# Performance work log

Hardware: AMD Instinct MI355X
Metric: run time of the kernel (lower is better)

Reference implementation:

```python
import jax, jax.numpy as jnp
import numpy as np

B, K, U = 4096, 512, 3
P, LIFT, HID, NSUB = 5, 32, 128, 10
RATE_LO, RATE_HI = 0.01, 3.0
BASAL_LO, BASAL_HI = 0.0, 0.3


def _xavier(key, shape):
    fan_in, fan_out = shape[1], shape[0]
    lim = np.sqrt(6.0 / (fan_in + fan_out))
    return jax.random.uniform(key, shape, jnp.float32, -lim, lim)


def setup_inputs() -> dict:
    key = jax.random.key(0)
    ks = jax.random.split(key, 10)
    return {
        "y0": jax.random.uniform(ks[0], (B, P), jnp.float32),
        "u_seq": jax.random.uniform(ks[1], (B, K, U), jnp.float32),
        "dt_seq": jax.random.uniform(ks[2], (B, K), jnp.float32),
        # lift: Linear(in_u+P -> LIFT)
        "Wl": _xavier(ks[3], (LIFT, U + P)),
        "bl": jnp.zeros((LIFT,), jnp.float32),
        # GRU (single layer): weight_ih (3H, LIFT), weight_hh (3H, H)
        "W_ih": _xavier(ks[4], (3 * HID, LIFT)),
        "b_ih": jnp.zeros((3 * HID,), jnp.float32),
        "W_hh": _xavier(ks[5], (3 * HID, HID)),
        "b_hh": jnp.zeros((3 * HID,), jnp.float32),
        # head: Linear(H -> 13)
        "Wh": _xavier(ks[6], (13, HID)),
        "bh": jnp.zeros((13,), jnp.float32),
        # bolus-to-state jump matrix (in_u, P)
        "u_to_y_jump": 0.1 * jax.random.uniform(ks[7], (U, P), jnp.float32),
    }


def _rhs(y, theta):
    # y: (B,5) [A,D,G,J,M]; theta: (B,13) [kf1..4, kr1..4, kj1..5]
    A, D, G, J, M = (y[:, i] for i in range(5))
    kf1, kf2, kf3, kf4, kr1, kr2, kr3, kr4, kj1, kj2, kj3, kj4, kj5 = (
        theta[:, i] for i in range(13))
    dA = -kf1 * A + kr1 * D + kj1
    dD = kf1 * A - kr1 * D - kf2 * D + kr2 * G + kj2
    dG = kf2 * D - kr2 * G - kf3 * G + kr3 * J + kj3
    dJ = kf3 * G - kr3 * J - kf4 * J + kr4 * M + kj4
    dM = kf4 * J - kr4 * M + kj5
    return jnp.stack([dA, dD, dG, dJ, dM], axis=-1)


def _rk4(y, h, theta):
    # h: (B,1) substep size
    k1 = _rhs(y, theta)
    k2 = _rhs(y + 0.5 * h * k1, theta)
    k3 = _rhs(y + 0.5 * h * k2, theta)
    k4 = _rhs(y + h * k3, theta)
    return jnp.maximum(y + h / 6.0 * (k1 + 2.0 * k2 + 2.0 * k3 + k4), 0.0)


def reference(y0, u_seq, dt_seq, Wl, bl, W_ih, b_ih, W_hh, b_hh, Wh, bh, u_to_y_jump):
    Bb = y0.shape[0]
    hid = W_hh.shape[1]

    def step(carry, inp):
        y_prev, hst = carry
        u_k, dt_k = inp  # (B,U), (B,)
        feat = jnp.concatenate([u_k, jax.lax.stop_gradient(y_prev)], axis=-1)
        x = jax.nn.silu(feat @ Wl.T + bl)
        # PyTorch GRUCell math
        gx = x @ W_ih.T + b_ih
        gh = hst @ W_hh.T + b_hh
        gxr, gxz, gxn = jnp.split(gx, 3, axis=-1)
        ghr, ghz, ghn = jnp.split(gh, 3, axis=-1)
        r = jax.nn.sigmoid(gxr + ghr)
        zg = jax.nn.sigmoid(gxz + ghz)
        n = jnp.tanh(gxn + r * ghn)
        h_new = (1.0 - zg) * n + zg * hst
        raw = h_new @ Wh.T + bh
        rates = RATE_LO + (RATE_HI - RATE_LO) * jax.nn.sigmoid(raw[:, 0:8])
        basal = BASAL_LO + (BASAL_HI - BASAL_LO) * jax.nn.sigmoid(raw[:, 8:13])
        theta = jnp.concatenate([rates, basal], axis=-1)
        y = y_prev + u_k @ u_to_y_jump
        hsub = (dt_k / float(NSUB))[:, None]
        for _ in range(NSUB):
            y = _rk4(y, hsub, theta)
        return (y, h_new), (y, theta)

    y_init = y0 + 0.01
    h0 = jnp.zeros((Bb, hid), dtype=y0.dtype)
    # scan over time: (K,B,...)
    _, (ys, thetas) = jax.lax.scan(
        step, (y_init, h0), (u_seq.transpose(1, 0, 2), dt_seq.T))
    y_out = ys.transpose(1, 0, 2)        # (B,K,P)
    theta_out = thetas.transpose(1, 0, 2)  # (B,K,13)
    return y_out, theta_out
```

## Files before the change

kernel.cpp:

```cpp
#include <hip/hip_runtime.h>
#include <cstdint>
#include <cstddef>


#define KTOT 512
#define BB   16

typedef _Float16 half8 __attribute__((ext_vector_type(8)));
typedef float    f32x4 __attribute__((ext_vector_type(4)));

struct __align__(16) Smem {
  _Float16 hf16[BB][136];
  _Float16 xls[BB][32];
  float yring[2][BB][16][5];
  float thring[2][BB][16][13];
  float brz[256];
  float bnx[128];
  float bnh[128];
  float bhv[16];
  float yst[BB][8];
  float ust[2][BB][4];
  float dtst[2][BB];
};

__device__ __forceinline__ float sigm(float x)     { return 1.f / (1.f + __expf(-x)); }
__device__ __forceinline__ float tanhfast(float x) { return 1.f - 2.f / (1.f + __expf(2.f * x)); }

template<int CTRL>
__device__ __forceinline__ float dppf(float x) {
  return __int_as_float(__builtin_amdgcn_mov_dpp(__float_as_int(x), CTRL, 0xf, 0xf, true));
}
#define QP_PLUS  0x39
#define QP_MINUS 0x93
#define QB0 0x00
#define QB1 0x55
#define QB2 0xAA
#define QB3 0xFF

#define MATMUL(Yr, Y4r, Xr, X4r, ALPHA) do {                                  \
  float xm_[5], xp_[5];                                                       \
  _Pragma("unroll")                                                           \
  for (int j_ = 0; j_ < 5; j_++) {                                            \
    xm_[j_] = dppf<QP_MINUS>(Xr[j_]);                                         \
    xp_[j_] = dppf<QP_PLUS >(Xr[j_]);                                         \
  }                                                                           \
  _Pragma("unroll")                                                           \
  for (int j_ = 0; j_ < 5; j_++) {                                            \
    const float ac_ = Zl*xm_[j_] + Zd*Xr[j_] + Zu*xp_[j_] + Zu4*X4r[j_];      \
    const float a4_ = Z43*Xr[j_] + Z44*X4r[j_];                               \
    Yr[j_]  = ((j_ == s_) ? 1.f : 0.f) + (ALPHA)*ac_;                         \
    Y4r[j_] = ((j_ == 4 ) ? 1.f : 0.f) + (ALPHA)*a4_;                         \
  } } while (0)

__global__ __launch_bounds__(512, 2) void rnn_scan_kernel(
    const float* __restrict__ y0,    const float* __restrict__ u_seq,
    const float* __restrict__ dt_sq, const float* __restrict__ Wl,
    const float* __restrict__ bl,    const float* __restrict__ W_ih,
    const float* __restrict__ b_ih,  const float* __restrict__ W_hh,
    const float* __restrict__ b_hh,  const float* __restrict__ Wh,
    const float* __restrict__ bh,    const float* __restrict__ jmp,
    float* __restrict__ y_out, float* __restrict__ th_out)
{
  __shared__ Smem sm;
  const int t   = threadIdx.x;
  const int w   = t >> 6;
  const int l   = t & 63;
  const int n16 = l & 15;
  const int q   = l >> 4;
  const int B0  = blockIdx.x * BB;

  if (t < 256) sm.brz[t] = b_ih[t] + b_hh[t];
  if (t < 128) { sm.bnx[t] = b_ih[256+t]; sm.bnh[t] = b_hh[256+t]; }
  if (t < 16)  sm.bhv[t] = (t < 13) ? bh[t] : 0.f;
  if (t >= 256 && t < 384) { const int b = (t-256) >> 3, i = (t-256) & 7;
    sm.yst[b][i] = (i < 5) ? (y0[(size_t)(B0+b)*5 + i] + 0.01f) : 0.f; }
  if (t >= 384 && t < 432) { const int idx = t-384, b = idx/3, c = idx - (idx/3)*3;
    sm.ust[0][b][c] = u_seq[((size_t)(B0+b)*KTOT + 0)*3 + c]; }
  if (t >= 432 && t < 448) sm.dtst[0][t-432] = dt_sq[(size_t)(B0+(t-432))*KTOT + 0];

  const int lb = t >> 5;
  const int lo = t & 31;
  float wlc[8];
  #pragma unroll
  for (int c = 0; c < 8; c++) wlc[c] = Wl[lo*8 + c];
  const float blv = bl[lo];

  half8 whf[4];
  #pragma unroll
  for (int ks = 0; ks < 4; ks++)
    #pragma unroll
    for (int i = 0; i < 8; i++) {
      const int kk = ks*32 + q*8 + i;
      whf[ks][i] = (n16 < 13) ? (_Float16)Wh[n16*128 + kk] : (_Float16)0.f;
    }

  const int jR = w*16 + n16;
  const int jZ = jR + 128, jN = jR + 256;
  half8 wihR, wihZ, wihN, whhR[4], whhZ[4], whhN[4];
  #pragma unroll
  for (int i = 0; i < 8; i++) {
    const int kk = q*8 + i;
    wihR[i] = (_Float16)W_ih[jR*32 + kk];
    wihZ[i] = (_Float16)W_ih[jZ*32 + kk];
    wihN[i] = (_Float16)W_ih[jN*32 + kk];
  }
  #pragma unroll
  for (int ks = 0; ks < 4; ks++)
    #pragma unroll
    for (int i = 0; i < 8; i++) {
      const int kk = ks*32 + q*8 + i;
      whhR[ks][i] = (_Float16)W_hh[jR*128 + kk];
      whhZ[ks][i] = (_Float16)W_hh[jZ*128 + kk];
      whhN[ks][i] = (_Float16)W_hh[jN*128 + kk];
    }

  float hreg[4] = {0.f, 0.f, 0.f, 0.f};
  const f32x4 zero4 = {0.f, 0.f, 0.f, 0.f};
  f32x4 accPreR = zero4, accPreZ = zero4, accPreN = zero4;

  const int s_ = l & 3, b4 = l >> 2;
  const float jr0 = jmp[0*5 + s_], jr1 = jmp[1*5 + s_], jr2 = jmp[2*5 + s_];
  const float j40 = (s_==3) ? jmp[4]  : 0.f;
  const float j41 = (s_==3) ? jmp[9]  : 0.f;
  const float j42 = (s_==3) ? jmp[14] : 0.f;

  const int upb = l/3, upc = l - (l/3)*3;

  __syncthreads();

  const float br  = sm.brz[jR];
  const float bz  = sm.brz[128 + jR];
  const float bx  = sm.bnx[jR];
  const float bn  = sm.bnh[jR];
  const float bb_ = sm.bhv[n16];

  #pragma unroll 1
  for (int k = 0; k < KTOT; k++) {
    const int buf  = k & 1;
    const int nbuf = (k + 1) & 1;
    const int kp   = (k + 1 < KTOT) ? (k + 1) : (KTOT - 1);

    {
      const f32x4 uu = *(const f32x4*)&sm.ust[buf][lb][0];
      const f32x4 ya = *(const f32x4*)&sm.yst[lb][0];
      const f32x4 yc = *(const f32x4*)&sm.yst[lb][4];
      const float a = blv
        + uu[0]*wlc[0] + uu[1]*wlc[1] + uu[2]*wlc[2]
        + ya[0]*wlc[3] + ya[1]*wlc[4] + ya[2]*wlc[5] + ya[3]*wlc[6]
        + yc[0]*wlc[7];
      sm.xls[lb][lo] = (_Float16)(a * sigm(a));
    }
    __syncthreads();

    {
      const half8 xf = *(const half8*)&sm.xls[n16][q*8];
      const f32x4 accR  = __builtin_amdgcn_mfma_f32_16x16x32_f16(xf, wihR, accPreR, 0,0,0);
      const f32x4 accZ  = __builtin_amdgcn_mfma_f32_16x16x32_f16(xf, wihZ, accPreZ, 0,0,0);
      const f32x4 accXN = __builtin_amdgcn_mfma_f32_16x16x32_f16(xf, wihN, zero4,   0,0,0);
      #pragma unroll
      for (int rg = 0; rg < 4; rg++) {
        const float r  = sigm(accR[rg] + br);
        const float z  = sigm(accZ[rg] + bz);
        const float nn = tanhfast(accXN[rg] + bx + r*(accPreN[rg] + bn));
        const float ho = hreg[rg];
        const float hn = nn + z*(ho - nn);
        hreg[rg] = hn;
        sm.hf16[q*4 + rg][jR] = (_Float16)hn;
      }
    }
    __syncthreads();

    float pref_u = 0.f, pref_dt = 0.f;
    if (w == 1 && l < 48)
      pref_u = u_seq[((size_t)(B0 + upb)*KTOT + kp)*3 + upc];
    if (w == 2 && l < 16)
      pref_dt = dt_sq[(size_t)(B0 + l)*KTOT + kp];

    half8 hfrag[4];
    #pragma unroll
    for (int ks = 0; ks < 4; ks++)
      hfrag[ks] = *(const half8*)&sm.hf16[n16][ks*32 + q*8];

    accPreR = zero4; accPreZ = zero4; accPreN = zero4;
    #pragma unroll
    for (int ks = 0; ks < 4; ks++) {
      accPreR = __builtin_amdgcn_mfma_f32_16x16x32_f16(hfrag[ks], whhR[ks], accPreR, 0,0,0);
      accPreZ = __builtin_amdgcn_mfma_f32_16x16x32_f16(hfrag[ks], whhZ[ks], accPreZ, 0,0,0);
      accPreN = __builtin_amdgcn_mfma_f32_16x16x32_f16(hfrag[ks], whhN[ks], accPreN, 0,0,0);
    }

    if (w == 0) {
      const int km = k & 15, hh = (k >> 4) & 1;
      f32x4 accH = zero4;
      #pragma unroll
      for (int ks = 0; ks < 4; ks++)
        accH = __builtin_amdgcn_mfma_f32_16x16x32_f16(hfrag[ks], whf[ks], accH, 0,0,0);
      #pragma unroll
      for (int rg = 0; rg < 4; rg++) {
        const float sg  = sigm(accH[rg] + bb_);
        const float thv = (n16 < 8) ? (0.01f + 2.99f*sg) : (0.3f*sg);
        if (n16 < 13) sm.thring[hh][q*4 + rg][km][n16] = thv;
      }
      const float* th = &sm.thring[hh][b4][km][0];
      const float dt = sm.dtst[buf][b4];
      const float h  = dt * 0.1f;
      const float thm = th[s_ ? (s_ - 1) : 0];
      const float Zl  = s_ ? h*thm : 0.f;
      const float krs = s_ ? th[3 + s_] : 0.f;
      const float Zd  = -h*(th[s_] + krs);
      const float Zur = h*th[4 + s_];
      const float Zu  = (s_ < 3) ? Zur : 0.f;
      const float Zu4 = (s_ == 3) ? Zur : 0.f;
      const float Z43 = h*th[3];
      const float Z44 = -h*th[7];
      const float c0 = th[8], c1 = th[9], c2 = th[10], c3 = th[11], c4 = th[12];
      float Xa[5], Xa4[5], Xb[5], Xb4[5];
      #pragma unroll
      for (int j = 0; j < 5; j++) {
        const float zr = (j == s_) ? Zd : ((j == s_ + 1) ? Zur : ((j + 1 == s_) ? Zl : 0.f));
        Xa[j] = ((j == s_) ? 1.f : 0.f) + 0.25f*zr;
      }
      Xa4[0] = 0.f; Xa4[1] = 0.f; Xa4[2] = 0.f;
      Xa4[3] = 0.25f*Z43; Xa4[4] = 1.f + 0.25f*Z44;
      MATMUL(Xb, Xb4, Xa, Xa4, (1.f/3.f));
      MATMUL(Xa, Xa4, Xb, Xb4, 0.5f);
      const float bv  = h*(Xa[0]*c0 + Xa[1]*c1 + Xa[2]*c2 + Xa[3]*c3 + Xa[4]*c4);
      const float bv4 = h*(Xa4[0]*c0 + Xa4[1]*c1 + Xa4[2]*c2 + Xa4[3]*c3 + Xa4[4]*c4);
      MATMUL(Xb, Xb4, Xa, Xa4, 1.f);
      const float uu0 = sm.ust[buf][b4][0], uu1 = sm.ust[buf][b4][1], uu2 = sm.ust[buf][b4][2];
      float y  = sm.yst[b4][s_] + uu0*jr0 + uu1*jr1 + uu2*jr2;
      float y4 = sm.yst[b4][4]  + uu0*j40 + uu1*j41 + uu2*j42;
      #pragma unroll
      for (int ss = 0; ss < 10; ss++) {
        const float v0 = dppf<QB0>(y), v1 = dppf<QB1>(y),
                    v2 = dppf<QB2>(y), v3 = dppf<QB3>(y);
        const float v4 = dppf<QB3>(y4);
        const float a1 = fmaf(Xb[0],  v0, bv);
        const float a2 = fmaf(Xb[2],  v2, Xb[1]*v1);
        const float a3 = fmaf(Xb[4],  v4, Xb[3]*v3);
        const float b1 = fmaf(Xb4[0], v0, bv4);
        const float b2 = fmaf(Xb4[2], v2, Xb4[1]*v1);
        const float b3 = fmaf(Xb4[4], v4, Xb4[3]*v3);
        const float yn  = fmaxf(a1 + (a2 + a3), 0.f);
        const float y4n = fmaxf(b1 + (b2 + b3), 0.f);
        y = yn; y4 = y4n;
      }
      sm.yst[b4][s_] = y;
      sm.yring[hh][b4][km][s_] = y;
      if (s_ == 3) { sm.yst[b4][4] = y4; sm.yring[hh][b4][km][4] = y4; }
    } else {
      if ((k & 15) == 0 && k >= 16) {
        const int hf = ((k >> 4) & 1) ^ 1;
        const int kb = k - 16;
        const int idx = t - 64;
        #pragma unroll
        for (int rep = 0; rep < 3; rep++) {
          const int o = idx + rep*448;
          if (o < 1152) {
            if (o < 320) {
              const int b = o/20, j = o - b*20;
              *(f32x4*)&y_out[((size_t)(B0 + b)*KTOT + kb)*5 + j*4] =
                  *(const f32x4*)((const float*)&sm.yring[hf][b][0][0] + j*4);
            } else {
              const int o2 = o - 320;
              const int b = o2/52, j = o2 - b*52;
              *(f32x4*)&th_out[((size_t)(B0 + b)*KTOT + kb)*13 + j*4] =
                  *(const f32x4*)((const float*)&sm.thring[hf][b][0][0] + j*4);
            }
          }
        }
      }
    }
    if (w == 1 && l < 48) sm.ust[nbuf][upb][upc] = pref_u;
    if (w == 2 && l < 16) sm.dtst[nbuf][l] = pref_dt;
    __syncthreads();
  }

  {
    const int kb = KTOT - 16;
    const int hf = ((KTOT >> 4) & 1) ^ 1;
    #pragma unroll
    for (int rep = 0; rep < 3; rep++) {
      const int o = t + rep*512;
      if (o < 1152) {
        if (o < 320) {
          const int b = o/20, j = o - b*20;
          *(f32x4*)&y_out[((size_t)(B0 + b)*KTOT + kb)*5 + j*4] =
              *(const f32x4*)((const float*)&sm.yring[hf][b][0][0] + j*4);
        } else {
          const int o2 = o - 320;
          const int b = o2/52, j = o2 - b*52;
          *(f32x4*)&th_out[((size_t)(B0 + b)*KTOT + kb)*13 + j*4] =
              *(const f32x4*)((const float*)&sm.thring[hf][b][0][0] + j*4);
        }
      }
    }
  }
}

extern "C" void kernel_launch(void* const* d_in, const int* in_sizes, int n_in,
                              void* d_out, int out_size, void* d_ws, size_t ws_size,
                              hipStream_t stream) {
  const float* y0     = (const float*)d_in[0];
  const float* u_seq  = (const float*)d_in[1];
  const float* dt_sq  = (const float*)d_in[2];
  const float* Wl     = (const float*)d_in[3];
  const float* bl     = (const float*)d_in[4];
  const float* W_ih   = (const float*)d_in[5];
  const float* b_ih   = (const float*)d_in[6];
  const float* W_hh   = (const float*)d_in[7];
  const float* b_hh   = (const float*)d_in[8];
  const float* Wh     = (const float*)d_in[9];
  const float* bh     = (const float*)d_in[10];
  const float* jmp    = (const float*)d_in[11];
  float* y_out  = (float*)d_out;
  float* th_out = y_out + (size_t)4096 * KTOT * 5;
  rnn_scan_kernel<<<256, 512, 0, stream>>>(
      y0, u_seq, dt_sq, Wl, bl, W_ih, b_ih, W_hh, b_hh, Wh, bh, jmp, y_out, th_out);
}
```

Measured before the change: 1.374 ms.

## Fuse lift layer into ODE wave to drop one barrier per timestep

The lift/SiLU computation for the next step moves into wave 0 right after the RK4 integration. The u-dependent part is precomputed into shared memory by all threads during the gate phase, and wave 0 keeps y in registers instead of a shared yst buffer. This removes one __syncthreads per timestep from the 512-step serial loop. The u/dt prefetch becomes a three-slot ring and the theta head MFMA chain is split into two accumulators. In exchange, wave 0 carries more serial work and more registers, which could lengthen the critical path.

```diff
diff --git a/kernel.cpp b/kernel.cpp
--- a/kernel.cpp
+++ b/kernel.cpp
@@ -12,15 +12,15 @@
 struct __align__(16) Smem {
   _Float16 hf16[BB][136];
   _Float16 xls[BB][32];
+  float au[BB][32];
   float yring[2][BB][16][5];
   float thring[2][BB][16][13];
   float brz[256];
   float bnx[128];
   float bnh[128];
   float bhv[16];
-  float yst[BB][8];
-  float ust[2][BB][4];
-  float dtst[2][BB];
+  float ust[3][BB][4];
+  float dtst[3][BB];
 };
 
 __device__ __forceinline__ float sigm(float x)     { return 1.f / (1.f + __expf(-x)); }
@@ -72,11 +72,13 @@
   if (t < 256) sm.brz[t] = b_ih[t] + b_hh[t];
   if (t < 128) { sm.bnx[t] = b_ih[256+t]; sm.bnh[t] = b_hh[256+t]; }
   if (t < 16)  sm.bhv[t] = (t < 13) ? bh[t] : 0.f;
-  if (t >= 256 && t < 384) { const int b = (t-256) >> 3, i = (t-256) & 7;
-    sm.yst[b][i] = (i < 5) ? (y0[(size_t)(B0+b)*5 + i] + 0.01f) : 0.f; }
-  if (t >= 384 && t < 432) { const int idx = t-384, b = idx/3, c = idx - (idx/3)*3;
-    sm.ust[0][b][c] = u_seq[((size_t)(B0+b)*KTOT + 0)*3 + c]; }
-  if (t >= 432 && t < 448) sm.dtst[0][t-432] = dt_sq[(size_t)(B0+(t-432))*KTOT + 0];
+  if (t >= 256 && t < 336) { const int b = (t-256)/5, i = (t-256) - ((t-256)/5)*5;
+    sm.yring[0][b][0][i] = y0[(size_t)(B0+b)*5 + i] + 0.01f; }
+  if (t >= 384 && t < 480) { const int idx = t-384, st = idx/48;
+    const int r = idx - st*48, b = r/3, c = r - (r/3)*3;
+    sm.ust[st][b][c] = u_seq[((size_t)(B0+b)*KTOT + st)*3 + c]; }
+  if (t >= 480) { const int idx = t-480, st = idx >> 4, b = idx & 15;
+    sm.dtst[st][b] = dt_sq[(size_t)(B0+b)*KTOT + st]; }
 
   const int lb = t >> 5;
   const int lo = t & 31;
@@ -84,6 +86,20 @@
   #pragma unroll
   for (int c = 0; c < 8; c++) wlc[c] = Wl[lo*8 + c];
   const float blv = bl[lo];
+
+  const int s_ = l & 3, b4 = l >> 2;
+  float wlyv[5][8];
+  #pragma unroll
+  for (int j = 0; j < 5; j++)
+    #pragma unroll
+    for (int i = 0; i < 8; i++) wlyv[j][i] = Wl[(s_*8 + i)*8 + 3 + j];
+  const float jr0 = jmp[0*5 + s_], jr1 = jmp[1*5 + s_], jr2 = jmp[2*5 + s_];
+  const float j40 = (s_==3) ? jmp[4]  : 0.f;
+  const float j41 = (s_==3) ? jmp[9]  : 0.f;
+  const float j42 = (s_==3) ? jmp[14] : 0.f;
+
+  float y  = y0[(size_t)(B0+b4)*5 + s_] + 0.01f;
+  float y4 = (s_==3) ? (y0[(size_t)(B0+b4)*5 + 4] + 0.01f) : 0.f;
 
   half8 whf[4];
   #pragma unroll
@@ -118,45 +134,40 @@
   const f32x4 zero4 = {0.f, 0.f, 0.f, 0.f};
   f32x4 accPreR = zero4, accPreZ = zero4, accPreN = zero4;
 
-  const int s_ = l & 3, b4 = l >> 2;
-  const float jr0 = jmp[0*5 + s_], jr1 = jmp[1*5 + s_], jr2 = jmp[2*5 + s_];
-  const float j40 = (s_==3) ? jmp[4]  : 0.f;
-  const float j41 = (s_==3) ? jmp[9]  : 0.f;
-  const float j42 = (s_==3) ? jmp[14] : 0.f;
-
   const int upb = l/3, upc = l - (l/3)*3;
 
   __syncthreads();
 
+  {
+    const f32x4 uu = *(const f32x4*)&sm.ust[0][lb][0];
+    const f32x4 ya = *(const f32x4*)&sm.yring[0][lb][0][0];
+    const float y4i = sm.yring[0][lb][0][4];
+    const float a = blv
+      + uu[0]*wlc[0] + uu[1]*wlc[1] + uu[2]*wlc[2]
+      + ya[0]*wlc[3] + ya[1]*wlc[4] + ya[2]*wlc[5] + ya[3]*wlc[6]
+      + y4i*wlc[7];
+    sm.xls[lb][lo] = (_Float16)(a * sigm(a));
+  }
   const float br  = sm.brz[jR];
   const float bz  = sm.brz[128 + jR];
   const float bx  = sm.bnx[jR];
   const float bn  = sm.bnh[jR];
   const float bb_ = sm.bhv[n16];
+  __syncthreads();
 
   #pragma unroll 1
   for (int k = 0; k < KTOT; k++) {
-    const int buf  = k & 1;
-    const int nbuf = (k + 1) & 1;
-    const int kp   = (k + 1 < KTOT) ? (k + 1) : (KTOT - 1);
-
-    {
-      const f32x4 uu = *(const f32x4*)&sm.ust[buf][lb][0];
-      const f32x4 ya = *(const f32x4*)&sm.yst[lb][0];
-      const f32x4 yc = *(const f32x4*)&sm.yst[lb][4];
-      const float a = blv
-        + uu[0]*wlc[0] + uu[1]*wlc[1] + uu[2]*wlc[2]
-        + ya[0]*wlc[3] + ya[1]*wlc[4] + ya[2]*wlc[5] + ya[3]*wlc[6]
-        + yc[0]*wlc[7];
-      sm.xls[lb][lo] = (_Float16)(a * sigm(a));
-    }
-    __syncthreads();
+    const int kp2 = (k + 2 < KTOT) ? (k + 2) : (KTOT - 1);
 
     {
       const half8 xf = *(const half8*)&sm.xls[n16][q*8];
       const f32x4 accR  = __builtin_amdgcn_mfma_f32_16x16x32_f16(xf, wihR, accPreR, 0,0,0);
       const f32x4 accZ  = __builtin_amdgcn_mfma_f32_16x16x32_f16(xf, wihZ, accPreZ, 0,0,0);
       const f32x4 accXN = __builtin_amdgcn_mfma_f32_16x16x32_f16(xf, wihN, zero4,   0,0,0);
+      {
+        const f32x4 uu = *(const f32x4*)&sm.ust[(k+1)%3][lb][0];
+        sm.au[lb][lo] = blv + uu[0]*wlc[0] + uu[1]*wlc[1] + uu[2]*wlc[2];
+      }
       #pragma unroll
       for (int rg = 0; rg < 4; rg++) {
         const float r  = sigm(accR[rg] + br);
@@ -172,9 +183,9 @@
 
     float pref_u = 0.f, pref_dt = 0.f;
     if (w == 1 && l < 48)
-      pref_u = u_seq[((size_t)(B0 + upb)*KTOT + kp)*3 + upc];
+      pref_u = u_seq[((size_t)(B0 + upb)*KTOT + kp2)*3 + upc];
     if (w == 2 && l < 16)
-      pref_dt = dt_sq[(size_t)(B0 + l)*KTOT + kp];
+      pref_dt = dt_sq[(size_t)(B0 + l)*KTOT + kp2];
 
     half8 hfrag[4];
     #pragma unroll
@@ -191,10 +202,13 @@
 
     if (w == 0) {
       const int km = k & 15, hh = (k >> 4) & 1;
-      f32x4 accH = zero4;
-      #pragma unroll
-      for (int ks = 0; ks < 4; ks++)
-        accH = __builtin_amdgcn_mfma_f32_16x16x32_f16(hfrag[ks], whf[ks], accH, 0,0,0);
+      const f32x4 au0 = *(const f32x4*)&sm.au[b4][s_*8];
+      const f32x4 au1 = *(const f32x4*)&sm.au[b4][s_*8 + 4];
+      f32x4 accHa = __builtin_amdgcn_mfma_f32_16x16x32_f16(hfrag[0], whf[0], zero4, 0,0,0);
+      f32x4 accHb = __builtin_amdgcn_mfma_f32_16x16x32_f16(hfrag[2], whf[2], zero4, 0,0,0);
+      accHa = __builtin_amdgcn_mfma_f32_16x16x32_f16(hfrag[1], whf[1], accHa, 0,0,0);
+      accHb = __builtin_amdgcn_mfma_f32_16x16x32_f16(hfrag[3], whf[3], accHb, 0,0,0);
+      const f32x4 accH = accHa + accHb;
       #pragma unroll
       for (int rg = 0; rg < 4; rg++) {
         const float sg  = sigm(accH[rg] + bb_);
@@ -202,7 +216,7 @@
         if (n16 < 13) sm.thring[hh][q*4 + rg][km][n16] = thv;
       }
       const float* th = &sm.thring[hh][b4][km][0];
-      const float dt = sm.dtst[buf][b4];
+      const float dt = sm.dtst[k%3][b4];
       const float h  = dt * 0.1f;
       const float thm = th[s_ ? (s_ - 1) : 0];
       const float Zl  = s_ ? h*thm : 0.f;
@@ -227,9 +241,9 @@
       const float bv  = h*(Xa[0]*c0 + Xa[1]*c1 + Xa[2]*c2 + Xa[3]*c3 + Xa[4]*c4);
       const float bv4 = h*(Xa4[0]*c0 + Xa4[1]*c1 + Xa4[2]*c2 + Xa4[3]*c3 + Xa4[4]*c4);
       MATMUL(Xb, Xb4, Xa, Xa4, 1.f);
-      const float uu0 = sm.ust[buf][b4][0], uu1 = sm.ust[buf][b4][1], uu2 = sm.ust[buf][b4][2];
-      float y  = sm.yst[b4][s_] + uu0*jr0 + uu1*jr1 + uu2*jr2;
-      float y4 = sm.yst[b4][4]  + uu0*j40 + uu1*j41 + uu2*j42;
+      const float uu0 = sm.ust[k%3][b4][0], uu1 = sm.ust[k%3][b4][1], uu2 = sm.ust[k%3][b4][2];
+      y  += uu0*jr0 + uu1*jr1 + uu2*jr2;
+      y4 += uu0*j40 + uu1*j41 + uu2*j42;
       #pragma unroll
       for (int ss = 0; ss < 10; ss++) {
         const float v0 = dppf<QB0>(y), v1 = dppf<QB1>(y),
@@ -241,13 +255,25 @@
         const float b1 = fmaf(Xb4[0], v0, bv4);
         const float b2 = fmaf(Xb4[2], v2, Xb4[1]*v1);
         const float b3 = fmaf(Xb4[4], v4, Xb4[3]*v3);
-        const float yn  = fmaxf(a1 + (a2 + a3), 0.f);
-        const float y4n = fmaxf(b1 + (b2 + b3), 0.f);
-        y = yn; y4 = y4n;
-      }
-      sm.yst[b4][s_] = y;
+        y  = fmaxf(a1 + (a2 + a3), 0.f);
+        y4 = fmaxf(b1 + (b2 + b3), 0.f);
+      }
       sm.yring[hh][b4][km][s_] = y;
-      if (s_ == 3) { sm.yst[b4][4] = y4; sm.yring[hh][b4][km][4] = y4; }
+      if (s_ == 3) sm.yring[hh][b4][km][4] = y4;
+      {
+        const float v0 = dppf<QB0>(y), v1 = dppf<QB1>(y),
+                    v2 = dppf<QB2>(y), v3 = dppf<QB3>(y);
+        const float v4 = dppf<QB3>(y4);
+        half8 xv;
+        #pragma unroll
+        for (int i = 0; i < 8; i++) {
+          const float aui = (i < 4) ? au0[i] : au1[i-4];
+          const float a = aui + v0*wlyv[0][i] + v1*wlyv[1][i] + v2*wlyv[2][i]
+                              + v3*wlyv[3][i] + v4*wlyv[4][i];
+          xv[i] = (_Float16)(a * sigm(a));
+        }
+        *(half8*)&sm.xls[b4][s_*8] = xv;
+      }
     } else {
       if ((k & 15) == 0 && k >= 16) {
         const int hf = ((k >> 4) & 1) ^ 1;
@@ -258,12 +284,12 @@
           const int o = idx + rep*448;
           if (o < 1152) {
             if (o < 320) {
-              const int b = o/20, j = o - b*20;
+              const int b = o/20, j = o - (o/20)*20;
               *(f32x4*)&y_out[((size_t)(B0 + b)*KTOT + kb)*5 + j*4] =
                   *(const f32x4*)((const float*)&sm.yring[hf][b][0][0] + j*4);
             } else {
               const int o2 = o - 320;
-              const int b = o2/52, j = o2 - b*52;
+              const int b = o2/52, j = o2 - (o2/52)*52;
               *(f32x4*)&th_out[((size_t)(B0 + b)*KTOT + kb)*13 + j*4] =
                   *(const f32x4*)((const float*)&sm.thring[hf][b][0][0] + j*4);
             }
@@ -271,25 +297,25 @@
         }
       }
     }
-    if (w == 1 && l < 48) sm.ust[nbuf][upb][upc] = pref_u;
-    if (w == 2 && l < 16) sm.dtst[nbuf][l] = pref_dt;
+    if (w == 1 && l < 48) sm.ust[(k+2)%3][upb][upc] = pref_u;
+    if (w == 2 && l < 16) sm.dtst[(k+2)%3][l] = pref_dt;
     __syncthreads();
   }
 
   {
     const int kb = KTOT - 16;
-    const int hf = ((KTOT >> 4) & 1) ^ 1;
+    const int hf = 1;
     #pragma unroll
     for (int rep = 0; rep < 3; rep++) {
       const int o = t + rep*512;
       if (o < 1152) {
         if (o < 320) {
-          const int b = o/20, j = o - b*20;
+          const int b = o/20, j = o - (o/20)*20;
           *(f32x4*)&y_out[((size_t)(B0 + b)*KTOT + kb)*5 + j*4] =
               *(const f32x4*)((const float*)&sm.yring[hf][b][0][0] + j*4);
         } else {
           const int o2 = o - 320;
-          const int b = o2/52, j = o2 - b*52;
+          const int b = o2/52, j = o2 - (o2/52)*52;
           *(f32x4*)&th_out[((size_t)(B0 + b)*KTOT + kb)*13 + j*4] =
               *(const f32x4*)((const float*)&sm.thring[hf][b][0][0] + j*4);
         }
```

Result: slower. 1.443 ms (+5.1%).

## Split head and RK4 integration across two waves and raise their priority

Applied to the files above, without the earlier changes.

The per-step head MFMA, the theta sigmoid and the RK4 substep chain were all done by wave 0. They are now split across waves 0 and 1: each wave computes the head and integrates 8 batch rows using its first 32 lanes. The head MFMAs are issued before the W_hh MFMAs, and these waves run at raised scheduling priority via s_setprio, to shorten the serial critical path before the barrier. Input prefetch and output stores move to the other waves. In exchange, both waves now compute the head MFMA redundantly, and half the lanes of each ODE wave sit idle.

```diff
diff --git a/kernel.cpp b/kernel.cpp
--- a/kernel.cpp
+++ b/kernel.cpp
@@ -118,7 +118,8 @@
   const f32x4 zero4 = {0.f, 0.f, 0.f, 0.f};
   f32x4 accPreR = zero4, accPreZ = zero4, accPreN = zero4;
 
-  const int s_ = l & 3, b4 = l >> 2;
+  const int s_ = l & 3;
+  const int b4w = (l >> 2) + w*8;
   const float jr0 = jmp[0*5 + s_], jr1 = jmp[1*5 + s_], jr2 = jmp[2*5 + s_];
   const float j40 = (s_==3) ? jmp[4]  : 0.f;
   const float j41 = (s_==3) ? jmp[9]  : 0.f;
@@ -170,16 +171,34 @@
     }
     __syncthreads();
 
+    const int km = k & 15, hh = (k >> 4) & 1;
     float pref_u = 0.f, pref_dt = 0.f;
-    if (w == 1 && l < 48)
+    if (w == 2 && l < 48)
       pref_u = u_seq[((size_t)(B0 + upb)*KTOT + kp)*3 + upc];
-    if (w == 2 && l < 16)
+    if (w == 3 && l < 16)
       pref_dt = dt_sq[(size_t)(B0 + l)*KTOT + kp];
 
     half8 hfrag[4];
     #pragma unroll
     for (int ks = 0; ks < 4; ks++)
       hfrag[ks] = *(const half8*)&sm.hf16[n16][ks*32 + q*8];
+
+    if (w < 2) {
+      __builtin_amdgcn_s_setprio(1);
+      f32x4 accHa = __builtin_amdgcn_mfma_f32_16x16x32_f16(hfrag[0], whf[0], zero4, 0,0,0);
+      f32x4 accHb = __builtin_amdgcn_mfma_f32_16x16x32_f16(hfrag[2], whf[2], zero4, 0,0,0);
+      accHa = __builtin_amdgcn_mfma_f32_16x16x32_f16(hfrag[1], whf[1], accHa, 0,0,0);
+      accHb = __builtin_amdgcn_mfma_f32_16x16x32_f16(hfrag[3], whf[3], accHb, 0,0,0);
+      const f32x4 accH = accHa + accHb;
+      if ((q >> 1) == w) {
+        #pragma unroll
+        for (int rg = 0; rg < 4; rg++) {
+          const float sg  = sigm(accH[rg] + bb_);
+          const float thv = (n16 < 8) ? (0.01f + 2.99f*sg) : (0.3f*sg);
+          if (n16 < 13) sm.thring[hh][q*4 + rg][km][n16] = thv;
+        }
+      }
+    }
 
     accPreR = zero4; accPreZ = zero4; accPreN = zero4;
     #pragma unroll
@@ -189,81 +208,72 @@
       accPreN = __builtin_amdgcn_mfma_f32_16x16x32_f16(hfrag[ks], whhN[ks], accPreN, 0,0,0);
     }
 
-    if (w == 0) {
-      const int km = k & 15, hh = (k >> 4) & 1;
-      f32x4 accH = zero4;
-      #pragma unroll
-      for (int ks = 0; ks < 4; ks++)
-        accH = __builtin_amdgcn_mfma_f32_16x16x32_f16(hfrag[ks], whf[ks], accH, 0,0,0);
-      #pragma unroll
-      for (int rg = 0; rg < 4; rg++) {
-        const float sg  = sigm(accH[rg] + bb_);
-        const float thv = (n16 < 8) ? (0.01f + 2.99f*sg) : (0.3f*sg);
-        if (n16 < 13) sm.thring[hh][q*4 + rg][km][n16] = thv;
-      }
-      const float* th = &sm.thring[hh][b4][km][0];
-      const float dt = sm.dtst[buf][b4];
-      const float h  = dt * 0.1f;
-      const float thm = th[s_ ? (s_ - 1) : 0];
-      const float Zl  = s_ ? h*thm : 0.f;
-      const float krs = s_ ? th[3 + s_] : 0.f;
-      const float Zd  = -h*(th[s_] + krs);
-      const float Zur = h*th[4 + s_];
-      const float Zu  = (s_ < 3) ? Zur : 0.f;
-      const float Zu4 = (s_ == 3) ? Zur : 0.f;
-      const float Z43 = h*th[3];
-      const float Z44 = -h*th[7];
-      const float c0 = th[8], c1 = th[9], c2 = th[10], c3 = th[11], c4 = th[12];
-      float Xa[5], Xa4[5], Xb[5], Xb4[5];
-      #pragma unroll
-      for (int j = 0; j < 5; j++) {
-        const float zr = (j == s_) ? Zd : ((j == s_ + 1) ? Zur : ((j + 1 == s_) ? Zl : 0.f));
-        Xa[j] = ((j == s_) ? 1.f : 0.f) + 0.25f*zr;
-      }
-      Xa4[0] = 0.f; Xa4[1] = 0.f; Xa4[2] = 0.f;
-      Xa4[3] = 0.25f*Z43; Xa4[4] = 1.f + 0.25f*Z44;
-      MATMUL(Xb, Xb4, Xa, Xa4, (1.f/3.f));
-      MATMUL(Xa, Xa4, Xb, Xb4, 0.5f);
-      const float bv  = h*(Xa[0]*c0 + Xa[1]*c1 + Xa[2]*c2 + Xa[3]*c3 + Xa[4]*c4);
-      const float bv4 = h*(Xa4[0]*c0 + Xa4[1]*c1 + Xa4[2]*c2 + Xa4[3]*c3 + Xa4[4]*c4);
-      MATMUL(Xb, Xb4, Xa, Xa4, 1.f);
-      const float uu0 = sm.ust[buf][b4][0], uu1 = sm.ust[buf][b4][1], uu2 = sm.ust[buf][b4][2];
-      float y  = sm.yst[b4][s_] + uu0*jr0 + uu1*jr1 + uu2*jr2;
-      float y4 = sm.yst[b4][4]  + uu0*j40 + uu1*j41 + uu2*j42;
-      #pragma unroll
-      for (int ss = 0; ss < 10; ss++) {
-        const float v0 = dppf<QB0>(y), v1 = dppf<QB1>(y),
-                    v2 = dppf<QB2>(y), v3 = dppf<QB3>(y);
-        const float v4 = dppf<QB3>(y4);
-        const float a1 = fmaf(Xb[0],  v0, bv);
-        const float a2 = fmaf(Xb[2],  v2, Xb[1]*v1);
-        const float a3 = fmaf(Xb[4],  v4, Xb[3]*v3);
-        const float b1 = fmaf(Xb4[0], v0, bv4);
-        const float b2 = fmaf(Xb4[2], v2, Xb4[1]*v1);
-        const float b3 = fmaf(Xb4[4], v4, Xb4[3]*v3);
-        const float yn  = fmaxf(a1 + (a2 + a3), 0.f);
-        const float y4n = fmaxf(b1 + (b2 + b3), 0.f);
-        y = yn; y4 = y4n;
-      }
-      sm.yst[b4][s_] = y;
-      sm.yring[hh][b4][km][s_] = y;
-      if (s_ == 3) { sm.yst[b4][4] = y4; sm.yring[hh][b4][km][4] = y4; }
-    } else {
+    if (w < 2) {
+      if (l < 32) {
+        const float* th = &sm.thring[hh][b4w][km][0];
+        const float dt = sm.dtst[buf][b4w];
+        const float h  = dt * 0.1f;
+        const float thm = th[s_ ? (s_ - 1) : 0];
+        const float Zl  = s_ ? h*thm : 0.f;
+        const float krs = s_ ? th[3 + s_] : 0.f;
+        const float Zd  = -h*(th[s_] + krs);
+        const float Zur = h*th[4 + s_];
+        const float Zu  = (s_ < 3) ? Zur : 0.f;
+        const float Zu4 = (s_ == 3) ? Zur : 0.f;
+        const float Z43 = h*th[3];
+        const float Z44 = -h*th[7];
+        const float c0 = th[8], c1 = th[9], c2 = th[10], c3 = th[11], c4 = th[12];
+        float Xa[5], Xa4[5], Xb[5], Xb4[5];
+        #pragma unroll
+        for (int j = 0; j < 5; j++) {
+          const float zr = (j == s_) ? Zd : ((j == s_ + 1) ? Zur : ((j + 1 == s_) ? Zl : 0.f));
+          Xa[j] = ((j == s_) ? 1.f : 0.f) + 0.25f*zr;
+        }
+        Xa4[0] = 0.f; Xa4[1] = 0.f; Xa4[2] = 0.f;
+        Xa4[3] = 0.25f*Z43; Xa4[4] = 1.f + 0.25f*Z44;
+        MATMUL(Xb, Xb4, Xa, Xa4, (1.f/3.f));
+        MATMUL(Xa, Xa4, Xb, Xb4, 0.5f);
+        const float bv  = h*(Xa[0]*c0 + Xa[1]*c1 + Xa[2]*c2 + Xa[3]*c3 + Xa[4]*c4);
+        const float bv4 = h*(Xa4[0]*c0 + Xa4[1]*c1 + Xa4[2]*c2 + Xa4[3]*c3 + Xa4[4]*c4);
+        MATMUL(Xb, Xb4, Xa, Xa4, 1.f);
+        const float uu0 = sm.ust[buf][b4w][0], uu1 = sm.ust[buf][b4w][1], uu2 = sm.ust[buf][b4w][2];
+        float y  = sm.yst[b4w][s_] + uu0*jr0 + uu1*jr1 + uu2*jr2;
+        float y4 = sm.yst[b4w][4]  + uu0*j40 + uu1*j41 + uu2*j42;
+        #pragma unroll
+        for (int ss = 0; ss < 10; ss++) {
+          const float v0 = dppf<QB0>(y), v1 = dppf<QB1>(y),
+                      v2 = dppf<QB2>(y), v3 = dppf<QB3>(y);
+          const float v4 = dppf<QB3>(y4);
+          const float a1 = fmaf(Xb[0],  v0, bv);
+          const float a2 = fmaf(Xb[2],  v2, Xb[1]*v1);
+          const float a3 = fmaf(Xb[4],  v4, Xb[3]*v3);
+          const float b1 = fmaf(Xb4[0], v0, bv4);
+          const float b2 = fmaf(Xb4[2], v2, Xb4[1]*v1);
+          const float b3 = fmaf(Xb4[4], v4, Xb4[3]*v3);
+          y  = fmaxf(a1 + (a2 + a3), 0.f);
+          y4 = fmaxf(b1 + (b2 + b3), 0.f);
+        }
+        sm.yst[b4w][s_] = y;
+        sm.yring[hh][b4w][km][s_] = y;
+        if (s_ == 3) { sm.yst[b4w][4] = y4; sm.yring[hh][b4w][km][4] = y4; }
+      }
+      __builtin_amdgcn_s_setprio(0);
+    } else if (w >= 4) {
       if ((k & 15) == 0 && k >= 16) {
-        const int hf = ((k >> 4) & 1) ^ 1;
+        const int hf = hh ^ 1;
         const int kb = k - 16;
-        const int idx = t - 64;
+        const int idx = t - 256;
         #pragma unroll
-        for (int rep = 0; rep < 3; rep++) {
-          const int o = idx + rep*448;
+        for (int rep = 0; rep < 5; rep++) {
+          const int o = idx + rep*256;
           if (o < 1152) {
             if (o < 320) {
-              const int b = o/20, j = o - b*20;
+              const int b = o/20, j = o - (o/20)*20;
               *(f32x4*)&y_out[((size_t)(B0 + b)*KTOT + kb)*5 + j*4] =
                   *(const f32x4*)((const float*)&sm.yring[hf][b][0][0] + j*4);
             } else {
               const int o2 = o - 320;
-              const int b = o2/52, j = o2 - b*52;
+              const int b = o2/52, j = o2 - (o2/52)*52;
               *(f32x4*)&th_out[((size_t)(B0 + b)*KTOT + kb)*13 + j*4] =
                   *(const f32x4*)((const float*)&sm.thring[hf][b][0][0] + j*4);
             }
@@ -271,25 +281,25 @@
         }
       }
     }
-    if (w == 1 && l < 48) sm.ust[nbuf][upb][upc] = pref_u;
-    if (w == 2 && l < 16) sm.dtst[nbuf][l] = pref_dt;
+    if (w == 2 && l < 48) sm.ust[nbuf][upb][upc] = pref_u;
+    if (w == 3 && l < 16) sm.dtst[nbuf][l] = pref_dt;
     __syncthreads();
   }
 
   {
     const int kb = KTOT - 16;
-    const int hf = ((KTOT >> 4) & 1) ^ 1;
+    const int hf = 1;
     #pragma unroll
     for (int rep = 0; rep < 3; rep++) {
       const int o = t + rep*512;
       if (o < 1152) {
         if (o < 320) {
-          const int b = o/20, j = o - b*20;
+          const int b = o/20, j = o - (o/20)*20;
           *(f32x4*)&y_out[((size_t)(B0 + b)*KTOT + kb)*5 + j*4] =
               *(const f32x4*)((const float*)&sm.yring[hf][b][0][0] + j*4);
         } else {
           const int o2 = o - 320;
-          const int b = o2/52, j = o2 - b*52;
+          const int b = o2/52, j = o2 - (o2/52)*52;
           *(f32x4*)&th_out[((size_t)(B0 + b)*KTOT + kb)*13 + j*4] =
               *(const f32x4*)((const float*)&sm.thring[hf][b][0][0] + j*4);
         }
```

New measurement: 1.426 ms. 1.04x slower.
